# Optimization experiments

Hardware: AMD Instinct MI355X
Metric: run time of the kernel (lower is better)

Reference implementation:

```python
import jax, jax.numpy as jnp
import numpy as np

B, C, W, H, HEADS = 32, 512, 32, 32, 8
D = C // HEADS
N = W * H
LN_EPS = 1e-5


def setup_inputs() -> dict:
    key = jax.random.key(0)
    ks = jax.random.split(key, 11)
    s = 1.0 / np.sqrt(C)
    return {
        "x": jax.random.normal(ks[0], (B, C, W, H), jnp.float32),
        "Wq": jax.random.normal(ks[1], (C, C), jnp.float32) * s,
        "bq": jax.random.normal(ks[2], (C,), jnp.float32) * 0.01,
        "Wk": jax.random.normal(ks[3], (C, C), jnp.float32) * s,
        "bk": jax.random.normal(ks[4], (C,), jnp.float32) * 0.01,
        "Wv": jax.random.normal(ks[5], (C, C), jnp.float32) * s,
        "bv": jax.random.normal(ks[6], (C,), jnp.float32) * 0.01,
        "rel_h": jax.random.normal(ks[7], (1, HEADS, D, 1, H), jnp.float32),
        "rel_w": jax.random.normal(ks[8], (1, HEADS, D, W, 1), jnp.float32),
        "ln_w": jnp.ones((C, W, H), jnp.float32),
        "ln_b": jnp.zeros((C, W, H), jnp.float32),
    }


def reference(x, Wq, bq, Wk, bk, Wv, bv, rel_h, rel_w, ln_w, ln_b):
    b, c, w, h = x.shape
    nh, d, n = HEADS, c // HEADS, w * h

    def proj(Wm, bm):
        # 1x1 conv == per-pixel linear: out[b,o,w,h] = sum_c Wm[o,c] x[b,c,w,h] + bm[o]
        y = jnp.einsum('bcwh,oc->bowh', x, Wm) + bm[None, :, None, None]
        return y.reshape(b, nh, d, n)

    q = proj(Wq, bq)  # [B,h,d,N]
    k = proj(Wk, bk)
    v = proj(Wv, bv)

    # content-content: q^T k -> [B,h,N,N]
    cc = jnp.einsum('bhdn,bhdm->bhnm', q, k)
    # content-position: (rel_h + rel_w) flattened to [h,d,N], permuted, matmul with q
    pos = (rel_h + rel_w).reshape(nh, d, n)  # [h,d,N]
    cp = jnp.einsum('hdn,bhdm->bhnm', pos, q)

    attn = jax.nn.softmax(cc + cp, axis=-1)  # [B,h,N,N]
    # out = v @ attn^T  -> [B,h,d,N]
    out = jnp.einsum('bhdn,bhmn->bhdm', v, attn)
    out = out.reshape(b, c, w, h)

    # LayerNorm over [C,W,H] with elementwise affine, then residual
    mu = jnp.mean(out, axis=(1, 2, 3), keepdims=True)
    var = jnp.var(out, axis=(1, 2, 3), keepdims=True)
    out = (out - mu) * jax.lax.rsqrt(var + LN_EPS) * ln_w[None] + ln_b[None]
    return out + x
```

## Files before the change

kernel.cpp:

```cpp
#include <hip/hip_runtime.h>
#include <stdint.h>

typedef _Float16 f16x8 __attribute__((ext_vector_type(8)));
typedef _Float16 f16x4 __attribute__((ext_vector_type(4)));
typedef __fp16   fp16x2 __attribute__((ext_vector_type(2)));
typedef float f32x4  __attribute__((ext_vector_type(4)));

__device__ __forceinline__ _Float16 f2h(float f){ return (_Float16)f; }

__device__ __forceinline__ void gl16(const void* g, void* l){
  __builtin_amdgcn_global_load_lds((const __attribute__((address_space(1))) void*)g,
                                   (__attribute__((address_space(3))) void*)l, 16, 0, 0);
}

#define NB   32
#define NC   512
#define NH   8
#define ND   64
#define NN   1024

#define LOG2E 1.44269504f

__global__ __launch_bounds__(256) void wt_conv(const float* __restrict__ Wq,
                                               const float* __restrict__ Wk,
                                               const float* __restrict__ Wv,
                                               _Float16* __restrict__ Wt){
  int idx = blockIdx.x * 256 + threadIdx.x;
  int sel = idx >> 18;
  const float* W = (sel == 0) ? Wq : (sel == 1) ? Wk : Wv;
  Wt[idx] = f2h(W[idx & 262143]);
}

__global__ __launch_bounds__(256) void transpose_x(const float* __restrict__ x,
                                                   _Float16* __restrict__ xT){
  __shared__ float tile[32][33];
  int n0 = blockIdx.x * 32, c0 = blockIdx.y * 32, b = blockIdx.z;
  int t = threadIdx.x;
  int tn = t & 31, tc = t >> 5;
#pragma unroll
  for (int k = 0; k < 4; k++)
    tile[tc + 8*k][tn] = x[(b*NC + c0 + tc + 8*k)*NN + n0 + tn];
  __syncthreads();
#pragma unroll
  for (int k = 0; k < 4; k++)
    xT[(b*NN + n0 + tc + 8*k)*NC + c0 + tn] = f2h(tile[tn][tc + 8*k]);
}

__global__ __launch_bounds__(256) void pos_conv(const float* __restrict__ rel_h,
                                                const float* __restrict__ rel_w,
                                                _Float16* __restrict__ pos_t){
  int idx = blockIdx.x * 256 + threadIdx.x;
  int d = idx & 63, n = (idx >> 6) & 1023, h = idx >> 16;
  int ww = n >> 5, hh = n & 31;
  float v = rel_h[(h*ND + d)*32 + hh] + rel_w[(h*ND + d)*32 + ww];
  pos_t[idx] = f2h(v);
}

#define TSTR 136

__global__ __launch_bounds__(256) void proj_gemm(const _Float16* __restrict__ Wt,
                                                 const _Float16* __restrict__ xT,
                                                 const float* __restrict__ bq,
                                                 const float* __restrict__ bk,
                                                 const float* __restrict__ bv,
                                                 _Float16* __restrict__ q_ws,
                                                 _Float16* __restrict__ k_ws,
                                                 _Float16* __restrict__ v_ws){
  __shared__ _Float16 smem[17408];
  _Float16* As = smem;
  _Float16* Bs = smem + 8192;

  int mt = blockIdx.x;
  int nt = blockIdx.y;
  int b  = blockIdx.z;
  int t = threadIdx.x, lane = t & 63, w = t >> 6;
  int wm = w >> 1, wn = w & 1;
  int lr = lane & 15, lg = lane >> 4;

  f32x4 acc[4][4];
#pragma unroll
  for (int i = 0; i < 4; i++)
#pragma unroll
    for (int j = 0; j < 4; j++) acc[i][j] = (f32x4)0.f;

  const _Float16* Arow = Wt + mt * 128 * NC;
  const _Float16* Brow = xT + (b * NN + nt * 128) * NC;

  int s_r8 = lane >> 3;
  int s_g  = lane & 7;

  for (int k0 = 0; k0 < NC; k0 += 64){
    __syncthreads();
#pragma unroll
    for (int i = 0; i < 4; i++){
      int r0  = w*32 + i*8;
      int row = r0 + s_r8;
      int gx  = (s_g ^ (row & 7)) << 3;
      gl16(Arow + row*NC + k0 + gx, As + r0*64);
      gl16(Brow + row*NC + k0 + gx, Bs + r0*64);
    }
    __syncthreads();
#pragma unroll
    for (int ks = 0; ks < 2; ks++){
      int xg = (((ks << 2) | lg) ^ (lr & 7)) << 3;
      f16x8 af[4], bfr[4];
#pragma unroll
      for (int mi = 0; mi < 4; mi++)
        af[mi] = *(f16x8*)(As + (wm*64 + mi*16 + lr)*64 + xg);
#pragma unroll
      for (int nj = 0; nj < 4; nj++)
        bfr[nj] = *(f16x8*)(Bs + (wn*64 + nj*16 + lr)*64 + xg);
      __builtin_amdgcn_s_setprio(1);
#pragma unroll
      for (int mi = 0; mi < 4; mi++)
#pragma unroll
        for (int nj = 0; nj < 4; nj++)
          acc[mi][nj] = __builtin_amdgcn_mfma_f32_16x16x32_f16(af[mi], bfr[nj], acc[mi][nj], 0, 0, 0);
      __builtin_amdgcn_s_setprio(0);
    }
  }
  __syncthreads();

  if (mt < 8){
    _Float16* Ts = smem;
#pragma unroll
    for (int mi = 0; mi < 4; mi++){
      int o0 = wm*64 + mi*16 + 4*lg;
      int og = mt*128 + o0;
      int sel = og >> 9, oo = og & 511;
      const float* bias = (sel == 0) ? bq : bk;
      float sc = (sel == 0) ? LOG2E : 1.f;
      float b0 = bias[oo], b1 = bias[oo+1], b2 = bias[oo+2], b3 = bias[oo+3];
#pragma unroll
      for (int nj = 0; nj < 4; nj++){
        int pix = wn*64 + nj*16 + lr;
        f16x4 pk;
        pk[0] = f2h((acc[mi][nj][0] + b0) * sc);
        pk[1] = f2h((acc[mi][nj][1] + b1) * sc);
        pk[2] = f2h((acc[mi][nj][2] + b2) * sc);
        pk[3] = f2h((acc[mi][nj][3] + b3) * sc);
        *(f16x4*)(Ts + pix*TSTR + o0) = pk;
      }
    }
    __syncthreads();
#pragma unroll
    for (int i = 0; i < 8; i++){
      int lin = t + 256 * i;
      int c_o = lin & 15, pix = lin >> 4;
      f16x8 v = *(f16x8*)(Ts + pix*TSTR + c_o*8);
      int og = mt*128 + c_o*8;
      int sel = og >> 9, oo = og & 511;
      int head = oo >> 6, d = oo & 63;
      _Float16* dst = (sel == 0) ? q_ws : k_ws;
      *(f16x8*)(dst + (((b*NH + head)*NN) + nt*128 + pix)*ND + d) = v;
    }
  } else {
    _Float16* Ts2 = smem;
#pragma unroll
    for (int mi = 0; mi < 4; mi++){
      int o0 = wm*64 + mi*16 + 4*lg;
      int vb = (mt - 8)*128 + o0;
      float b0 = bv[vb], b1 = bv[vb+1], b2 = bv[vb+2], b3 = bv[vb+3];
#pragma unroll
      for (int nj = 0; nj < 4; nj++){
        int pix = wn*64 + nj*16 + lr;
        Ts2[(o0+0)*TSTR + pix] = f2h(acc[mi][nj][0] + b0);
        Ts2[(o0+1)*TSTR + pix] = f2h(acc[mi][nj][1] + b1);
        Ts2[(o0+2)*TSTR + pix] = f2h(acc[mi][nj][2] + b2);
        Ts2[(o0+3)*TSTR + pix] = f2h(acc[mi][nj][3] + b3);
      }
    }
    __syncthreads();
#pragma unroll
    for (int i = 0; i < 8; i++){
      int lin = t + 256 * i;
      int pix8 = lin & 15, o_loc = lin >> 4;
      f16x8 v = *(f16x8*)(Ts2 + o_loc*TSTR + pix8*8);
      int vb = (mt - 8)*128 + o_loc;
      int head = vb >> 6, d = vb & 63;
      *(f16x8*)(v_ws + ((b*NH + head)*ND + d)*NN + nt*128 + pix8*8) = v;
    }
  }
}

#define KSTR 136
#define PSTR 72
#define OSTR 65
#define OFF_VT 8704
#define OFF_P  12800

__global__ __launch_bounds__(256, 3) void attn_kernel(const _Float16* __restrict__ q_ws,
                                                      const _Float16* __restrict__ k_ws,
                                                      const _Float16* __restrict__ v_ws,
                                                      const _Float16* __restrict__ pos_t,
                                                      float* __restrict__ out,
                                                      float* __restrict__ red){
  __shared__ _Float16 smem[22016];
  __shared__ float lnred[8];
  _Float16* Kc = smem;
  _Float16* Vt = smem + OFF_VT;
  _Float16* Pl = smem + OFF_P;

  int bid = blockIdx.x;
  int sid = (bid & 7) * 256 + (bid >> 3);
  int qt = sid & 7, h = (sid >> 3) & 7, b = sid >> 6;

  int t = threadIdx.x, lane = t & 63, w = t >> 6;
  int lr = lane & 15, lg = lane >> 4;

  const _Float16* qbh = q_ws + (b*NH + h) * NN * ND;
  const _Float16* kbh = k_ws + (b*NH + h) * NN * ND;
  const _Float16* vbh = v_ws + (b*NH + h) * ND * NN;
  const _Float16* pph = pos_t + h * NN * ND;

  f16x8 qreg[2][4];
#pragma unroll
  for (int qi = 0; qi < 2; qi++){
    int row = qt*128 + w*32 + qi*16 + lr;
#pragma unroll
    for (int ks = 0; ks < 4; ks++){
      const _Float16* src = (ks < 2) ? (qbh + row*ND + ks*32 + lg*8)
                                     : (pph + row*ND + (ks-2)*32 + lg*8);
      qreg[qi][ks] = *(const f16x8*)src;
    }
  }

  f16x8 ones;
#pragma unroll
  for (int e = 0; e < 8; e++) ones[e] = (_Float16)1.f;

  float m_r[2];
  f32x4 oacc[2][4];
  f32x4 lacc[2];
#pragma unroll
  for (int qi = 0; qi < 2; qi++){ m_r[qi] = -1e30f; lacc[qi] = (f32x4)0.f; }
#pragma unroll
  for (int qi = 0; qi < 2; qi++)
#pragma unroll
    for (int dj = 0; dj < 4; dj++) oacc[qi][dj] = (f32x4)0.f;

  for (int n0 = 0; n0 < NN; n0 += 64){
    __syncthreads();
#pragma unroll
    for (int i = 0; i < 4; i++){
      int lin = t + 256*i;
      int row = lin >> 4, c8 = lin & 15;
      const _Float16* src = (c8 < 8) ? (kbh + (n0 + row)*ND + c8*8)
                                     : (qbh + (n0 + row)*ND + (c8 - 8)*8);
      *(f16x8*)(Kc + row*KSTR + c8*8) = *(const f16x8*)src;
    }
#pragma unroll
    for (int i = 0; i < 2; i++){
      int lin = t + 256*i;
      int d = lin >> 3, ch = lin & 7;
      *(f16x8*)(Vt + d*64 + ((ch*8) ^ ((d & 7) << 3))) = *(const f16x8*)(vbh + d*NN + n0 + ch*8);
    }
    __syncthreads();

    f32x4 sacc[4][2];
#pragma unroll
    for (int kt = 0; kt < 4; kt++)
#pragma unroll
      for (int qi = 0; qi < 2; qi++) sacc[kt][qi] = (f32x4)0.f;
    __builtin_amdgcn_s_setprio(1);
#pragma unroll
    for (int ks = 0; ks < 4; ks++){
      f16x8 kf[4];
#pragma unroll
      for (int kt = 0; kt < 4; kt++)
        kf[kt] = *(f16x8*)(Kc + (kt*16 + lr)*KSTR + ks*32 + lg*8);
#pragma unroll
      for (int kt = 0; kt < 4; kt++)
#pragma unroll
        for (int qi = 0; qi < 2; qi++)
          sacc[kt][qi] = __builtin_amdgcn_mfma_f32_16x16x32_f16(kf[kt], qreg[qi][ks], sacc[kt][qi], 0, 0, 0);
    }
    __builtin_amdgcn_s_setprio(0);

#pragma unroll
    for (int qi = 0; qi < 2; qi++){
      float m0 = fmaxf(fmaxf(sacc[0][qi][0], sacc[0][qi][1]), fmaxf(sacc[0][qi][2], sacc[0][qi][3]));
      float m1 = fmaxf(fmaxf(sacc[1][qi][0], sacc[1][qi][1]), fmaxf(sacc[1][qi][2], sacc[1][qi][3]));
      float m2 = fmaxf(fmaxf(sacc[2][qi][0], sacc[2][qi][1]), fmaxf(sacc[2][qi][2], sacc[2][qi][3]));
      float m3 = fmaxf(fmaxf(sacc[3][qi][0], sacc[3][qi][1]), fmaxf(sacc[3][qi][2], sacc[3][qi][3]));
      float mx = fmaxf(fmaxf(m0, m1), fmaxf(m2, m3));
      mx = fmaxf(mx, __shfl_xor(mx, 16));
      mx = fmaxf(mx, __shfl_xor(mx, 32));
      if (!__all(mx - m_r[qi] <= 11.f)){
        float mn2 = fmaxf(m_r[qi], mx);
        float cr = __builtin_exp2f(m_r[qi] - mn2);
        m_r[qi] = mn2;
#pragma unroll
        for (int r = 0; r < 4; r++){
          float crow = __shfl(cr, 4*lg + r);
          lacc[qi][r] *= crow;
#pragma unroll
          for (int dj = 0; dj < 4; dj++) oacc[qi][dj][r] *= crow;
        }
      }
      float mn = m_r[qi];
#pragma unroll
      for (int kt = 0; kt < 4; kt++){
        float p0 = __builtin_exp2f(sacc[kt][qi][0] - mn);
        float p1 = __builtin_exp2f(sacc[kt][qi][1] - mn);
        float p2 = __builtin_exp2f(sacc[kt][qi][2] - mn);
        float p3 = __builtin_exp2f(sacc[kt][qi][3] - mn);
        union { fp16x2 h2[2]; uint2 u2; } pu;
        pu.h2[0] = __builtin_amdgcn_cvt_pkrtz(p0, p1);
        pu.h2[1] = __builtin_amdgcn_cvt_pkrtz(p2, p3);
        *(uint2*)(Pl + (w*32 + qi*16 + lr)*PSTR + kt*16 + lg*4) = pu.u2;
      }
    }

    __builtin_amdgcn_s_setprio(1);
#pragma unroll
    for (int ks = 0; ks < 2; ks++){
      f16x8 pf[2], vf[4];
#pragma unroll
      for (int qi = 0; qi < 2; qi++)
        pf[qi] = *(f16x8*)(Pl + (w*32 + qi*16 + lr)*PSTR + ks*32 + lg*8);
#pragma unroll
      for (int dj = 0; dj < 4; dj++){
        int row = dj*16 + lr;
        vf[dj] = *(f16x8*)(Vt + row*64 + ((ks*32 + lg*8) ^ ((row & 7) << 3)));
      }
#pragma unroll
      for (int qi = 0; qi < 2; qi++){
        lacc[qi] = __builtin_amdgcn_mfma_f32_16x16x32_f16(pf[qi], ones, lacc[qi], 0, 0, 0);
#pragma unroll
        for (int dj = 0; dj < 4; dj++)
          oacc[qi][dj] = __builtin_amdgcn_mfma_f32_16x16x32_f16(pf[qi], vf[dj], oacc[qi][dj], 0, 0, 0);
      }
    }
    __builtin_amdgcn_s_setprio(0);
  }

  float s_ln = 0.f, q_ln = 0.f;
  __syncthreads();
  float* Ot = (float*)smem;
#pragma unroll
  for (int qi = 0; qi < 2; qi++){
#pragma unroll
    for (int r = 0; r < 4; r++){
      float invr = 1.f / lacc[qi][r];
#pragma unroll
      for (int dj = 0; dj < 4; dj++){
        float val = oacc[qi][dj][r] * invr;
        s_ln += val; q_ln += val*val;
        Ot[(w*32 + qi*16 + 4*lg + r)*OSTR + dj*16 + lr] = val;
      }
    }
  }
  __syncthreads();

#pragma unroll
  for (int i = 0; i < 8; i++){
    int lin = t + 256*i;
    int jc = lin & 31, d = lin >> 5;
    float4 v;
    v.x = Ot[(jc*4 + 0)*OSTR + d];
    v.y = Ot[(jc*4 + 1)*OSTR + d];
    v.z = Ot[(jc*4 + 2)*OSTR + d];
    v.w = Ot[(jc*4 + 3)*OSTR + d];
    *(float4*)(out + (b*NC + h*ND + d)*NN + qt*128 + jc*4) = v;
  }

#pragma unroll
  for (int off = 1; off < 64; off <<= 1){
    s_ln += __shfl_xor(s_ln, off);
    q_ln += __shfl_xor(q_ln, off);
  }
  if (lane == 0){ lnred[w*2] = s_ln; lnred[w*2 + 1] = q_ln; }
  __syncthreads();
  if (t == 0){
    int idx = ((b*NH + h)*8 + qt)*2;
    red[idx]     = lnred[0] + lnred[2] + lnred[4] + lnred[6];
    red[idx + 1] = lnred[1] + lnred[3] + lnred[5] + lnred[7];
  }
}

__global__ void ln_stats(const float* __restrict__ red, float* __restrict__ stats){
  int b = threadIdx.x;
  if (b < 32){
    float s = 0.f, sq = 0.f;
    for (int j = 0; j < 64; j++){ s += red[(b*64 + j)*2]; sq += red[(b*64 + j)*2 + 1]; }
    float mu  = s * (1.f / 524288.f);
    float var = sq * (1.f / 524288.f) - mu*mu;
    stats[b*2] = mu;
    stats[b*2 + 1] = rsqrtf(var + 1e-5f);
  }
}

__global__ __launch_bounds__(256) void ln_apply(const float* __restrict__ x,
                                                const float* __restrict__ lw,
                                                const float* __restrict__ lb,
                                                const float* __restrict__ stats,
                                                float* __restrict__ out){
  int tid = blockIdx.x*256 + threadIdx.x;
  for (int i4 = tid; i4 < 4194304; i4 += 524288){
    int b = i4 >> 17;
    int r4 = i4 & 131071;
    float mu = stats[b*2], rs = stats[b*2 + 1];
    float4 o  = ((const float4*)out)[i4];
    float4 xv = ((const float4*)x)[i4];
    float4 ww = ((const float4*)lw)[r4];
    float4 bb = ((const float4*)lb)[r4];
    o.x = (o.x - mu)*rs*ww.x + bb.x + xv.x;
    o.y = (o.y - mu)*rs*ww.y + bb.y + xv.y;
    o.z = (o.z - mu)*rs*ww.z + bb.z + xv.z;
    o.w = (o.w - mu)*rs*ww.w + bb.w + xv.w;
    ((float4*)out)[i4] = o;
  }
}

extern "C" void kernel_launch(void* const* d_in, const int* in_sizes, int n_in,
                              void* d_out, int out_size, void* d_ws, size_t ws_size,
                              hipStream_t stream){
  (void)in_sizes; (void)n_in; (void)out_size; (void)ws_size;
  const float* x    = (const float*)d_in[0];
  const float* Wq   = (const float*)d_in[1];
  const float* bq   = (const float*)d_in[2];
  const float* Wk   = (const float*)d_in[3];
  const float* bk   = (const float*)d_in[4];
  const float* Wv   = (const float*)d_in[5];
  const float* bv   = (const float*)d_in[6];
  const float* relh = (const float*)d_in[7];
  const float* relw = (const float*)d_in[8];
  const float* lnw  = (const float*)d_in[9];
  const float* lnb  = (const float*)d_in[10];
  float* out = (float*)d_out;
  char* ws = (char*)d_ws;

  _Float16* q_ws  = (_Float16*)(ws);
  _Float16* k_ws  = (_Float16*)(ws + 33554432);
  _Float16* v_ws  = (_Float16*)(ws + 67108864);
  _Float16* xT    = (_Float16*)(ws + 100663296);
  _Float16* Wt    = (_Float16*)(ws + 134217728);
  _Float16* pos_t = (_Float16*)(ws + 135790592);
  float* red   = (float*)(ws + 136839168);
  float* stats = red + 4096;

  wt_conv    <<<3072, 256, 0, stream>>>(Wq, Wk, Wv, Wt);
  transpose_x<<<dim3(32, 16, 32), 256, 0, stream>>>(x, xT);
  pos_conv   <<<2048, 256, 0, stream>>>(relh, relw, pos_t);
  proj_gemm  <<<dim3(12, 8, 32), 256, 0, stream>>>(Wt, xT, bq, bk, bv, q_ws, k_ws, v_ws);
  attn_kernel<<<2048, 256, 0, stream>>>(q_ws, k_ws, v_ws, pos_t, out, red);
  ln_stats   <<<1, 64, 0, stream>>>(red, stats);
  ln_apply   <<<2048, 256, 0, stream>>>(x, lnw, lnb, stats, out);
}
```

Before: 298.5 us.

## Split attention work across 8 waves per block with 16 query rows each

The attention kernel now launches 512 threads per block (8 wavefronts), and each wave owns 16 query rows instead of 32. This halves per-wave registers for score and output accumulators, adds waves per CU for latency hiding, and splits the K/V tile loads across more threads. In exchange, each K/V fragment read from LDS is reused by half as many query rows, so the ratio of LDS reads to MFMA work rises. The barriers also now synchronize twice as many waves.

```diff
diff --git a/kernel.cpp b/kernel.cpp
--- a/kernel.cpp
+++ b/kernel.cpp
@@ -189,14 +189,14 @@
 #define OFF_VT 8704
 #define OFF_P  12800
 
-__global__ __launch_bounds__(256, 3) void attn_kernel(const _Float16* __restrict__ q_ws,
+__global__ __launch_bounds__(512, 6) void attn_kernel(const _Float16* __restrict__ q_ws,
                                                       const _Float16* __restrict__ k_ws,
                                                       const _Float16* __restrict__ v_ws,
                                                       const _Float16* __restrict__ pos_t,
                                                       float* __restrict__ out,
                                                       float* __restrict__ red){
   __shared__ _Float16 smem[22016];
-  __shared__ float lnred[8];
+  __shared__ float lnred[16];
   _Float16* Kc = smem;
   _Float16* Vt = smem + OFF_VT;
   _Float16* Pl = smem + OFF_P;
@@ -213,15 +213,14 @@
   const _Float16* vbh = v_ws + (b*NH + h) * ND * NN;
   const _Float16* pph = pos_t + h * NN * ND;
 
-  f16x8 qreg[2][4];
-#pragma unroll
-  for (int qi = 0; qi < 2; qi++){
-    int row = qt*128 + w*32 + qi*16 + lr;
+  f16x8 qreg[4];
+  {
+    int row = qt*128 + w*16 + lr;
 #pragma unroll
     for (int ks = 0; ks < 4; ks++){
       const _Float16* src = (ks < 2) ? (qbh + row*ND + ks*32 + lg*8)
                                      : (pph + row*ND + (ks-2)*32 + lg*8);
-      qreg[qi][ks] = *(const f16x8*)src;
+      qreg[ks] = *(const f16x8*)src;
     }
   }
 
@@ -229,39 +228,31 @@
 #pragma unroll
   for (int e = 0; e < 8; e++) ones[e] = (_Float16)1.f;
 
-  float m_r[2];
-  f32x4 oacc[2][4];
-  f32x4 lacc[2];
-#pragma unroll
-  for (int qi = 0; qi < 2; qi++){ m_r[qi] = -1e30f; lacc[qi] = (f32x4)0.f; }
-#pragma unroll
-  for (int qi = 0; qi < 2; qi++)
-#pragma unroll
-    for (int dj = 0; dj < 4; dj++) oacc[qi][dj] = (f32x4)0.f;
+  float m_r = -1e30f;
+  f32x4 oacc[4];
+  f32x4 lacc = (f32x4)0.f;
+#pragma unroll
+  for (int dj = 0; dj < 4; dj++) oacc[dj] = (f32x4)0.f;
 
   for (int n0 = 0; n0 < NN; n0 += 64){
     __syncthreads();
 #pragma unroll
-    for (int i = 0; i < 4; i++){
-      int lin = t + 256*i;
+    for (int i = 0; i < 2; i++){
+      int lin = t + 512*i;
       int row = lin >> 4, c8 = lin & 15;
       const _Float16* src = (c8 < 8) ? (kbh + (n0 + row)*ND + c8*8)
                                      : (qbh + (n0 + row)*ND + (c8 - 8)*8);
       *(f16x8*)(Kc + row*KSTR + c8*8) = *(const f16x8*)src;
     }
-#pragma unroll
-    for (int i = 0; i < 2; i++){
-      int lin = t + 256*i;
-      int d = lin >> 3, ch = lin & 7;
+    {
+      int d = t >> 3, ch = t & 7;
       *(f16x8*)(Vt + d*64 + ((ch*8) ^ ((d & 7) << 3))) = *(const f16x8*)(vbh + d*NN + n0 + ch*8);
     }
     __syncthreads();
 
-    f32x4 sacc[4][2];
-#pragma unroll
-    for (int kt = 0; kt < 4; kt++)
-#pragma unroll
-      for (int qi = 0; qi < 2; qi++) sacc[kt][qi] = (f32x4)0.f;
+    f32x4 sacc[4];
+#pragma unroll
+    for (int kt = 0; kt < 4; kt++) sacc[kt] = (f32x4)0.f;
     __builtin_amdgcn_s_setprio(1);
 #pragma unroll
     for (int ks = 0; ks < 4; ks++){
@@ -271,66 +262,58 @@
         kf[kt] = *(f16x8*)(Kc + (kt*16 + lr)*KSTR + ks*32 + lg*8);
 #pragma unroll
       for (int kt = 0; kt < 4; kt++)
-#pragma unroll
-        for (int qi = 0; qi < 2; qi++)
-          sacc[kt][qi] = __builtin_amdgcn_mfma_f32_16x16x32_f16(kf[kt], qreg[qi][ks], sacc[kt][qi], 0, 0, 0);
+        sacc[kt] = __builtin_amdgcn_mfma_f32_16x16x32_f16(kf[kt], qreg[ks], sacc[kt], 0, 0, 0);
     }
     __builtin_amdgcn_s_setprio(0);
 
-#pragma unroll
-    for (int qi = 0; qi < 2; qi++){
-      float m0 = fmaxf(fmaxf(sacc[0][qi][0], sacc[0][qi][1]), fmaxf(sacc[0][qi][2], sacc[0][qi][3]));
-      float m1 = fmaxf(fmaxf(sacc[1][qi][0], sacc[1][qi][1]), fmaxf(sacc[1][qi][2], sacc[1][qi][3]));
-      float m2 = fmaxf(fmaxf(sacc[2][qi][0], sacc[2][qi][1]), fmaxf(sacc[2][qi][2], sacc[2][qi][3]));
-      float m3 = fmaxf(fmaxf(sacc[3][qi][0], sacc[3][qi][1]), fmaxf(sacc[3][qi][2], sacc[3][qi][3]));
+    {
+      float m0 = fmaxf(fmaxf(sacc[0][0], sacc[0][1]), fmaxf(sacc[0][2], sacc[0][3]));
+      float m1 = fmaxf(fmaxf(sacc[1][0], sacc[1][1]), fmaxf(sacc[1][2], sacc[1][3]));
+      float m2 = fmaxf(fmaxf(sacc[2][0], sacc[2][1]), fmaxf(sacc[2][2], sacc[2][3]));
+      float m3 = fmaxf(fmaxf(sacc[3][0], sacc[3][1]), fmaxf(sacc[3][2], sacc[3][3]));
       float mx = fmaxf(fmaxf(m0, m1), fmaxf(m2, m3));
       mx = fmaxf(mx, __shfl_xor(mx, 16));
       mx = fmaxf(mx, __shfl_xor(mx, 32));
-      if (!__all(mx - m_r[qi] <= 11.f)){
-        float mn2 = fmaxf(m_r[qi], mx);
-        float cr = __builtin_exp2f(m_r[qi] - mn2);
-        m_r[qi] = mn2;
+      if (!__all(mx - m_r <= 11.f)){
+        float mn2 = fmaxf(m_r, mx);
+        float cr = __builtin_exp2f(m_r - mn2);
+        m_r = mn2;
 #pragma unroll
         for (int r = 0; r < 4; r++){
           float crow = __shfl(cr, 4*lg + r);
-          lacc[qi][r] *= crow;
-#pragma unroll
-          for (int dj = 0; dj < 4; dj++) oacc[qi][dj][r] *= crow;
+          lacc[r] *= crow;
+#pragma unroll
+          for (int dj = 0; dj < 4; dj++) oacc[dj][r] *= crow;
         }
       }
-      float mn = m_r[qi];
+      float mn = m_r;
 #pragma unroll
       for (int kt = 0; kt < 4; kt++){
-        float p0 = __builtin_exp2f(sacc[kt][qi][0] - mn);
-        float p1 = __builtin_exp2f(sacc[kt][qi][1] - mn);
-        float p2 = __builtin_exp2f(sacc[kt][qi][2] - mn);
-        float p3 = __builtin_exp2f(sacc[kt][qi][3] - mn);
+        float p0 = __builtin_exp2f(sacc[kt][0] - mn);
+        float p1 = __builtin_exp2f(sacc[kt][1] - mn);
+        float p2 = __builtin_exp2f(sacc[kt][2] - mn);
+        float p3 = __builtin_exp2f(sacc[kt][3] - mn);
         union { fp16x2 h2[2]; uint2 u2; } pu;
         pu.h2[0] = __builtin_amdgcn_cvt_pkrtz(p0, p1);
         pu.h2[1] = __builtin_amdgcn_cvt_pkrtz(p2, p3);
-        *(uint2*)(Pl + (w*32 + qi*16 + lr)*PSTR + kt*16 + lg*4) = pu.u2;
+        *(uint2*)(Pl + (w*16 + lr)*PSTR + kt*16 + lg*4) = pu.u2;
       }
     }
 
     __builtin_amdgcn_s_setprio(1);
 #pragma unroll
     for (int ks = 0; ks < 2; ks++){
-      f16x8 pf[2], vf[4];
-#pragma unroll
-      for (int qi = 0; qi < 2; qi++)
-        pf[qi] = *(f16x8*)(Pl + (w*32 + qi*16 + lr)*PSTR + ks*32 + lg*8);
+      f16x8 pf, vf[4];
+      pf = *(f16x8*)(Pl + (w*16 + lr)*PSTR + ks*32 + lg*8);
 #pragma unroll
       for (int dj = 0; dj < 4; dj++){
         int row = dj*16 + lr;
         vf[dj] = *(f16x8*)(Vt + row*64 + ((ks*32 + lg*8) ^ ((row & 7) << 3)));
       }
-#pragma unroll
-      for (int qi = 0; qi < 2; qi++){
-        lacc[qi] = __builtin_amdgcn_mfma_f32_16x16x32_f16(pf[qi], ones, lacc[qi], 0, 0, 0);
-#pragma unroll
-        for (int dj = 0; dj < 4; dj++)
-          oacc[qi][dj] = __builtin_amdgcn_mfma_f32_16x16x32_f16(pf[qi], vf[dj], oacc[qi][dj], 0, 0, 0);
-      }
+      lacc = __builtin_amdgcn_mfma_f32_16x16x32_f16(pf, ones, lacc, 0, 0, 0);
+#pragma unroll
+      for (int dj = 0; dj < 4; dj++)
+        oacc[dj] = __builtin_amdgcn_mfma_f32_16x16x32_f16(pf, vf[dj], oacc[dj], 0, 0, 0);
     }
     __builtin_amdgcn_s_setprio(0);
   }
@@ -339,23 +322,20 @@
   __syncthreads();
   float* Ot = (float*)smem;
 #pragma unroll
-  for (int qi = 0; qi < 2; qi++){
-#pragma unroll
-    for (int r = 0; r < 4; r++){
-      float invr = 1.f / lacc[qi][r];
-#pragma unroll
-      for (int dj = 0; dj < 4; dj++){
-        float val = oacc[qi][dj][r] * invr;
-        s_ln += val; q_ln += val*val;
-        Ot[(w*32 + qi*16 + 4*lg + r)*OSTR + dj*16 + lr] = val;
-      }
+  for (int r = 0; r < 4; r++){
+    float invr = 1.f / lacc[r];
+#pragma unroll
+    for (int dj = 0; dj < 4; dj++){
+      float val = oacc[dj][r] * invr;
+      s_ln += val; q_ln += val*val;
+      Ot[(w*16 + 4*lg + r)*OSTR + dj*16 + lr] = val;
     }
   }
   __syncthreads();
 
 #pragma unroll
-  for (int i = 0; i < 8; i++){
-    int lin = t + 256*i;
+  for (int i = 0; i < 4; i++){
+    int lin = t + 512*i;
     int jc = lin & 31, d = lin >> 5;
     float4 v;
     v.x = Ot[(jc*4 + 0)*OSTR + d];
@@ -373,9 +353,12 @@
   if (lane == 0){ lnred[w*2] = s_ln; lnred[w*2 + 1] = q_ln; }
   __syncthreads();
   if (t == 0){
+    float rs = 0.f, rq = 0.f;
+#pragma unroll
+    for (int j = 0; j < 8; j++){ rs += lnred[j*2]; rq += lnred[j*2 + 1]; }
     int idx = ((b*NH + h)*8 + qt)*2;
-    red[idx]     = lnred[0] + lnred[2] + lnred[4] + lnred[6];
-    red[idx + 1] = lnred[1] + lnred[3] + lnred[5] + lnred[7];
+    red[idx]     = rs;
+    red[idx + 1] = rq;
   }
 }
 
@@ -444,7 +427,7 @@
   transpose_x<<<dim3(32, 16, 32), 256, 0, stream>>>(x, xT);
   pos_conv   <<<2048, 256, 0, stream>>>(relh, relw, pos_t);
   proj_gemm  <<<dim3(12, 8, 32), 256, 0, stream>>>(Wt, xT, bq, bk, bv, q_ws, k_ws, v_ws);
-  attn_kernel<<<2048, 256, 0, stream>>>(q_ws, k_ws, v_ws, pos_t, out, red);
+  attn_kernel<<<2048, 512, 0, stream>>>(q_ws, k_ws, v_ws, pos_t, out, red);
   ln_stats   <<<1, 64, 0, stream>>>(red, stats);
   ln_apply   <<<2048, 256, 0, stream>>>(x, lnw, lnb, stats, out);
 }
```

New measurement: 343.3 us. 1.15x slower.
